# Kernel optimization log

Hardware: AMD Instinct MI355X
Metric: run time of the kernel (lower is better)

The kernel has to match this reference:

```python
import jax, jax.numpy as jnp
import numpy as np

B, LQ, LK = 4, 512, 512
QS, KS, H, DV = 512, 512, 256, 512


def setup_inputs() -> dict:
    key = jax.random.key(0)
    ks = jax.random.split(key, 9)
    s_q = 1.0 / np.sqrt(QS)
    s_k = 1.0 / np.sqrt(KS)
    s_v = 1.0 / np.sqrt(H)
    return {
        "query": jax.random.normal(ks[0], (B, LQ, QS), jnp.float32),
        "key": jax.random.normal(ks[1], (B, LK, KS), jnp.float32),
        "value": jax.random.normal(ks[2], (B, LK, DV), jnp.float32),
        "wq": jax.random.uniform(ks[3], (H, QS), jnp.float32, -s_q, s_q),
        "bq": jax.random.uniform(ks[4], (H,), jnp.float32, -s_q, s_q),
        "wk": jax.random.uniform(ks[5], (H, KS), jnp.float32, -s_k, s_k),
        "bk": jax.random.uniform(ks[6], (H,), jnp.float32, -s_k, s_k),
        "wv": jax.random.uniform(ks[7], (H,), jnp.float32, -s_v, s_v),
        "bv": jax.random.uniform(ks[8], (), jnp.float32, -s_v, s_v),
    }


def reference(query, key, value, wq, bq, wk, bk, wv, bv):
    # q: [B, Lq, H], k: [B, Lk, H]
    q = jnp.einsum('bqd,hd->bqh', query, wq) + bq
    k = jnp.einsum('bkd,hd->bkh', key, wk) + bk
    # broadcast add -> [B, Lq, Lk, H], tanh, project to scalar score
    feats = jnp.tanh(q[:, :, None, :] + k[:, None, :, :])
    scores = jnp.einsum('bqkh,h->bqk', feats, wv) + bv  # [B, Lq, Lk]
    attn = jax.nn.softmax(scores, axis=-1)
    # dropout p=0.0 (identity at inference)
    return jnp.einsum('bqk,bkd->bqd', attn, value)
```

## Files before the change

### kernel.cpp

```cpp
#include <hip/hip_runtime.h>

#define LOG2E 1.4426950408889634f

constexpr int Bb = 4, LQ = 512, LK = 512, QS = 512, H = 256, DV = 512;
constexpr int M = 2048;

constexpr size_t OFF_EQT = 0;
constexpr size_t OFF_EKT = 2u << 20;
constexpr size_t OFF_PQ  = 4u << 20;
constexpr size_t OFF_ROW = 6u << 20;
constexpr size_t OFF_VT  = 8u << 20;

using bf16x8 = __attribute__((ext_vector_type(8))) short;
using f32x4v = __attribute__((ext_vector_type(4))) float;

__device__ inline unsigned short f2bf(float x) {
    unsigned int u = __float_as_uint(x);
    u += 0x7FFFu + ((u >> 16) & 1u);
    return (unsigned short)(u >> 16);
}
__device__ inline unsigned int pk2(float lo, float hi) {
    unsigned int r;
    asm("v_cvt_pk_bf16_f32 %0, %1, %2" : "=v"(r) : "v"(lo), "v"(hi));
    return r;
}

__global__ __launch_bounds__(512) void proj_mfma(
    const float* __restrict__ query, const float* __restrict__ key,
    const float* __restrict__ wq, const float* __restrict__ wk,
    const float* __restrict__ bq, const float* __restrict__ bk,
    char* __restrict__ ws, float scale)
{
    const int z = blockIdx.z;
    const float* A    = z ? key : query;
    const float* W    = z ? wk : wq;
    const float* bias = z ? bk : bq;
    float* out = (float*)(ws + (z ? OFF_EKT : OFF_EQT));
    const float off = z ? 0.0f : 13.0f;

    __shared__ unsigned short Als[64][136];
    __shared__ unsigned short Wls[64][136];
    __shared__ float Ot[64][68];

    const int mb = blockIdx.x * 64, nb = blockIdx.y * 64;
    const int tid = threadIdx.x;
    const int wid = tid >> 6, lane = tid & 63;
    const int ml = lane & 15, quad = lane >> 4;
    const int ms = wid & 3, nh = wid >> 2;

    f32x4v acc0 = {0, 0, 0, 0}, acc1 = {0, 0, 0, 0};

    for (int kc = 0; kc < QS; kc += 128) {
        __syncthreads();
#pragma unroll
        for (int it = 0; it < 2; ++it) {
            int u = tid + it * 512;
            int row = u >> 4, c8 = (u & 15) * 8;
            float4 a0 = *(const float4*)(A + (size_t)(mb + row) * 512 + kc + c8);
            float4 a1 = *(const float4*)(A + (size_t)(mb + row) * 512 + kc + c8 + 4);
            uint4 pa = { pk2(a0.x, a0.y), pk2(a0.z, a0.w), pk2(a1.x, a1.y), pk2(a1.z, a1.w) };
            *(uint4*)&Als[row][c8] = pa;
            float4 w0 = *(const float4*)(W + (size_t)(nb + row) * 512 + kc + c8);
            float4 w1 = *(const float4*)(W + (size_t)(nb + row) * 512 + kc + c8 + 4);
            uint4 pw = { pk2(w0.x, w0.y), pk2(w0.z, w0.w), pk2(w1.x, w1.y), pk2(w1.z, w1.w) };
            *(uint4*)&Wls[row][c8] = pw;
        }
        __syncthreads();
#pragma unroll
        for (int s = 0; s < 4; ++s) {
            int k = s * 32 + quad * 8;
            bf16x8 af = *(const bf16x8*)&Als[ms * 16 + ml][k];
            bf16x8 b0 = *(const bf16x8*)&Wls[(nh * 2 + 0) * 16 + ml][k];
            bf16x8 b1 = *(const bf16x8*)&Wls[(nh * 2 + 1) * 16 + ml][k];
            acc0 = __builtin_amdgcn_mfma_f32_16x16x32_bf16(af, b0, acc0, 0, 0, 0);
            acc1 = __builtin_amdgcn_mfma_f32_16x16x32_bf16(af, b1, acc1, 0, 0, 0);
        }
    }

    __syncthreads();
#pragma unroll
    for (int r = 0; r < 4; ++r) {
        Ot[(nh * 2 + 0) * 16 + ml][ms * 16 + quad * 4 + r] = acc0[r];
        Ot[(nh * 2 + 1) * 16 + ml][ms * 16 + quad * 4 + r] = acc1[r];
    }
    __syncthreads();
    {
        int r0 = tid >> 3;
        int c0 = (tid & 7) * 8;
        float bs = bias[nb + r0];
#pragma unroll
        for (int g = 0; g < 2; ++g) {
            float4 v = *(const float4*)&Ot[r0][c0 + g * 4];
            float4 o;
            o.x = __builtin_amdgcn_exp2f(fminf(fmaxf(scale * (v.x + bs), -13.f), 13.f) - off);
            o.y = __builtin_amdgcn_exp2f(fminf(fmaxf(scale * (v.y + bs), -13.f), 13.f) - off);
            o.z = __builtin_amdgcn_exp2f(fminf(fmaxf(scale * (v.z + bs), -13.f), 13.f) - off);
            o.w = __builtin_amdgcn_exp2f(fminf(fmaxf(scale * (v.w + bs), -13.f), 13.f) - off);
            *(float4*)(out + (size_t)(nb + r0) * 2048 + mb + c0 + g * 4) = o;
        }
    }
}

__global__ __launch_bounds__(256) void vconv(
    const float* __restrict__ V, char* __restrict__ ws)
{
    unsigned short* VT = (unsigned short*)(ws + OFF_VT);
    __shared__ unsigned short T[64][72];
    const int b = blockIdx.z, k0 = blockIdx.x * 64, n0 = blockIdx.y * 64;
    const int tid = threadIdx.x;
    const float* Vb = V + (size_t)b * 512 * 512;
    const int r = tid >> 4, c = (tid & 15) * 4;
#pragma unroll
    for (int it = 0; it < 4; ++it) {
        int kr = r + it * 16;
        float4 v = *(const float4*)(Vb + (size_t)(k0 + kr) * 512 + n0 + c);
        T[c + 0][kr] = f2bf(v.x);
        T[c + 1][kr] = f2bf(v.y);
        T[c + 2][kr] = f2bf(v.z);
        T[c + 3][kr] = f2bf(v.w);
    }
    __syncthreads();
    const int rowO = tid >> 3, colO = (tid & 7) * 8;
#pragma unroll
    for (int it = 0; it < 2; ++it) {
        int n = rowO + it * 32;
        uint4 o = *(const uint4*)&T[n][colO];
        *(uint4*)(VT + ((size_t)b * 512 + n0 + n) * 512 + k0 + colO) = o;
    }
}

__global__ __launch_bounds__(512, 4) void score_kernel(
    const float* __restrict__ wvp, char* __restrict__ ws)
{
    const float* EqT = (const float*)(ws + OFF_EQT);
    const float* EkT = (const float*)(ws + OFF_EKT);
    unsigned short* Pq = (unsigned short*)(ws + OFF_PQ);
    float* rowpart = (float*)(ws + OFF_ROW);

    __shared__ float Qs[64][32];
    __shared__ float Ks[64][64];
    __shared__ float Wv2[H];
    __shared__ float redS[8][32];

    const int b  = blockIdx.z;
    const int qb = blockIdx.x * 32;
    const int kt = blockIdx.y;
    const int kb = kt * 64;
    const int tid = threadIdx.x;
    const int tx = tid & 15;
    const int ty = tid >> 4;
    const int w  = tid >> 6;
    const int lane = tid & 63;

    constexpr float S = 0.0001220703125f;
    if (tid < H) Wv2[tid] = wvp[tid] * (2.0f * LOG2E) * S;

    const int mq = b * LQ + qb;
    const int mk = b * LK + kb;

    float acc[2][2] = {};

    for (int h0 = 0; h0 < H; h0 += 64) {
        __syncthreads();
        {
            int hq = tid >> 3, cq = (tid & 7) * 4;
            *(float4*)&Qs[hq][cq] = *(const float4*)(EqT + (size_t)(h0 + hq) * M + mq + cq);
            int hk = tid >> 4, ck = (tid & 15) * 4;
            *(float4*)&Ks[hk][ck]      = *(const float4*)(EkT + (size_t)(h0 + hk) * M + mk + ck);
            *(float4*)&Ks[hk + 32][ck] = *(const float4*)(EkT + (size_t)(h0 + hk + 32) * M + mk + ck);
        }
        __syncthreads();
#pragma unroll 2
        for (int hh = 0; hh < 64; hh += 8) {
            float2 qv[8], kv[8];
#pragma unroll
            for (int u = 0; u < 8; ++u) qv[u] = *(const float2*)&Qs[hh + u][tx * 2];
#pragma unroll
            for (int u = 0; u < 8; ++u) kv[u] = *(const float2*)&Ks[hh + u][ty * 2];
            const float4 wA = *(const float4*)&Wv2[h0 + hh];
            const float4 wB = *(const float4*)&Wv2[h0 + hh + 4];
#pragma unroll
            for (int i = 0; i < 2; ++i)
#pragma unroll
                for (int j = 0; j < 2; ++j) {
                    float t[8];
#pragma unroll
                    for (int u = 0; u < 8; ++u)
                        t[u] = fmaf(i ? qv[u].y : qv[u].x, j ? kv[u].y : kv[u].x, S);
                    float t12 = t[0] * t[1], t34 = t[2] * t[3];
                    float n12 = fmaf(wA.x, t[1], wA.y * t[0]);
                    float n34 = fmaf(wA.z, t[3], wA.w * t[2]);
                    float numA = fmaf(n12, t34, n34 * t12);
                    float denA = t12 * t34;
                    float t56 = t[4] * t[5], t78 = t[6] * t[7];
                    float m12 = fmaf(wB.x, t[5], wB.y * t[4]);
                    float m34 = fmaf(wB.z, t[7], wB.w * t[6]);
                    float numB = fmaf(m12, t78, m34 * t56);
                    float denB = t56 * t78;
                    float NUMv = fmaf(numA, denB, numB * denA);
                    float DENv = denA * denB;
                    acc[i][j] = fmaf(NUMv, __builtin_amdgcn_rcpf(DENv), acc[i][j]);
                }
        }
    }

    float ps[2];
#pragma unroll
    for (int i = 0; i < 2; ++i) {
        int q = qb + tx * 2 + i;
        float p0 = __builtin_amdgcn_exp2f(-acc[i][0]);
        float p1 = __builtin_amdgcn_exp2f(-acc[i][1]);
        ps[i] = p0 + p1;
        *(unsigned int*)(Pq + ((size_t)(b * 512 + q) * 512 + kb + ty * 2)) = pk2(p0, p1);
    }
#pragma unroll
    for (int i = 0; i < 2; ++i) {
        ps[i] += __shfl_xor(ps[i], 16, 64);
        ps[i] += __shfl_xor(ps[i], 32, 64);
    }
    if (lane < 16) {
#pragma unroll
        for (int i = 0; i < 2; ++i) redS[w][tx * 2 + i] = ps[i];
    }
    __syncthreads();
    if (tid < 32) {
        float s = ((redS[0][tid] + redS[1][tid]) + (redS[2][tid] + redS[3][tid]))
                + ((redS[4][tid] + redS[5][tid]) + (redS[6][tid] + redS[7][tid]));
        rowpart[(size_t)kt * 2048 + b * 512 + qb + tid] = s;
    }
}

__global__ __launch_bounds__(512, 2) void av_mfma(
    const char* __restrict__ wsc, float* __restrict__ O)
{
    const unsigned short* Pq = (const unsigned short*)(wsc + OFF_PQ);
    const unsigned short* VT = (const unsigned short*)(wsc + OFF_VT);
    const float* rowpart = (const float*)(wsc + OFF_ROW);

    __shared__ unsigned short Pls[64][136];
    __shared__ unsigned short Vls[64][136];

    const int b = blockIdx.z, qb = blockIdx.x * 64, nb = blockIdx.y * 64;
    const int tid = threadIdx.x;
    const int wid = tid >> 6, lane = tid & 63;
    const int ml = lane & 15, quad = lane >> 4;
    const int ms = wid & 3, nh = wid >> 2;
    const unsigned short* Pb = Pq + (size_t)b * 512 * 512;
    const unsigned short* Vb = VT + (size_t)b * 512 * 512;

    f32x4v acc[2] = {{0,0,0,0},{0,0,0,0}};

    for (int kc = 0; kc < LK; kc += 128) {
        __syncthreads();
#pragma unroll
        for (int it = 0; it < 2; ++it) {
            int u = tid + it * 512;
            int row = u >> 4, c8 = (u & 15) * 8;
            *(uint4*)&Pls[row][c8] = *(const uint4*)(Pb + (size_t)(qb + row) * 512 + kc + c8);
            *(uint4*)&Vls[row][c8] = *(const uint4*)(Vb + (size_t)(nb + row) * 512 + kc + c8);
        }
        __syncthreads();
#pragma unroll
        for (int s = 0; s < 4; ++s) {
            int k = s * 32 + quad * 8;
            bf16x8 af = *(const bf16x8*)&Pls[ms * 16 + ml][k];
#pragma unroll
            for (int t = 0; t < 2; ++t) {
                bf16x8 bfr = *(const bf16x8*)&Vls[(nh * 2 + t) * 16 + ml][k];
                acc[t] = __builtin_amdgcn_mfma_f32_16x16x32_bf16(af, bfr, acc[t], 0, 0, 0);
            }
        }
    }

    float rr[4];
#pragma unroll
    for (int r = 0; r < 4; ++r) {
        int q = qb + ms * 16 + quad * 4 + r;
        float rs = 0.f;
#pragma unroll
        for (int t8 = 0; t8 < 8; ++t8) rs += rowpart[(size_t)t8 * 2048 + b * 512 + q];
        rr[r] = 1.0f / rs;
    }
#pragma unroll
    for (int t = 0; t < 2; ++t)
#pragma unroll
        for (int r = 0; r < 4; ++r) {
            int q = qb + ms * 16 + quad * 4 + r;
            O[((size_t)b * 512 + q) * 512 + nb + (nh * 2 + t) * 16 + ml] = acc[t][r] * rr[r];
        }
}

extern "C" void kernel_launch(void* const* d_in, const int* in_sizes, int n_in,
                              void* d_out, int out_size, void* d_ws, size_t ws_size,
                              hipStream_t stream) {
    const float* query = (const float*)d_in[0];
    const float* key   = (const float*)d_in[1];
    const float* value = (const float*)d_in[2];
    const float* wq    = (const float*)d_in[3];
    const float* bq    = (const float*)d_in[4];
    const float* wk    = (const float*)d_in[5];
    const float* bk    = (const float*)d_in[6];
    const float* wv    = (const float*)d_in[7];
    float* out = (float*)d_out;
    char* ws = (char*)d_ws;

    const float c2 = 2.0f * LOG2E;

    proj_mfma<<<dim3(32, 4, 2), 512, 0, stream>>>(query, key, wq, wk, bq, bk, ws, c2);
    vconv<<<dim3(8, 8, Bb), 256, 0, stream>>>(value, ws);
    score_kernel<<<dim3(16, 8, Bb), 512, 0, stream>>>(wv, ws);
    av_mfma<<<dim3(8, 8, Bb), 512, 0, stream>>>(ws, out);
}
```

Before: 118.4 us.

## Merge V conversion into projection kernel and prefetch tiles through registers

Folds the value transpose and bf16 conversion into the projection launch as a third grid slice, dropping one kernel launch. It also adds register prefetching of the next K-chunk in the projection and AV GEMM loops, plus double-buffered LDS with a register prefetch in the score kernel, so global loads overlap compute. The costs are higher register pressure, more LDS in the score kernel (which may lower occupancy), and a union-shared layout for the merged kernel.

```diff
diff --git a/kernel.cpp b/kernel.cpp
--- a/kernel.cpp
+++ b/kernel.cpp
@@ -25,63 +25,111 @@
     return r;
 }
 
-__global__ __launch_bounds__(512) void proj_mfma(
+__global__ __launch_bounds__(512, 4) void proj_vconv(
     const float* __restrict__ query, const float* __restrict__ key,
     const float* __restrict__ wq, const float* __restrict__ wk,
     const float* __restrict__ bq, const float* __restrict__ bk,
-    char* __restrict__ ws, float scale)
+    const float* __restrict__ V, char* __restrict__ ws, float scale)
 {
+    union Sh {
+        struct {
+            unsigned short Als[64][136];
+            unsigned short Wls[64][136];
+            float Ot[64][68];
+        } p;
+        unsigned short T[128][72];
+    };
+    __shared__ Sh sh;
+
+    const int tid = threadIdx.x;
     const int z = blockIdx.z;
+
+    if (z == 2) {
+        unsigned short* VT = (unsigned short*)(ws + OFF_VT);
+        const int id = blockIdx.y * 32 + blockIdx.x;
+        const int b = id >> 5;
+        const int t32 = id & 31;
+        const int k0 = (t32 & 7) * 64, n0 = (t32 >> 3) * 128;
+        const float* Vb = V + (size_t)b * 512 * 512;
+        const int r = tid >> 5, c = (tid & 31) * 4;
+#pragma unroll
+        for (int it = 0; it < 4; ++it) {
+            int kr = r + it * 16;
+            float4 v = *(const float4*)(Vb + (size_t)(k0 + kr) * 512 + n0 + c);
+            sh.T[c + 0][kr] = f2bf(v.x);
+            sh.T[c + 1][kr] = f2bf(v.y);
+            sh.T[c + 2][kr] = f2bf(v.z);
+            sh.T[c + 3][kr] = f2bf(v.w);
+        }
+        __syncthreads();
+        const int rowO = tid >> 2, colO = (tid & 3) * 16;
+        uint4 o0 = *(const uint4*)&sh.T[rowO][colO];
+        uint4 o1 = *(const uint4*)&sh.T[rowO][colO + 8];
+        unsigned short* dst = VT + ((size_t)b * 512 + n0 + rowO) * 512 + k0 + colO;
+        *(uint4*)(dst)     = o0;
+        *(uint4*)(dst + 8) = o1;
+        return;
+    }
+
     const float* A    = z ? key : query;
     const float* W    = z ? wk : wq;
     const float* bias = z ? bk : bq;
     float* out = (float*)(ws + (z ? OFF_EKT : OFF_EQT));
     const float off = z ? 0.0f : 13.0f;
 
-    __shared__ unsigned short Als[64][136];
-    __shared__ unsigned short Wls[64][136];
-    __shared__ float Ot[64][68];
-
     const int mb = blockIdx.x * 64, nb = blockIdx.y * 64;
-    const int tid = threadIdx.x;
     const int wid = tid >> 6, lane = tid & 63;
     const int ml = lane & 15, quad = lane >> 4;
     const int ms = wid & 3, nh = wid >> 2;
 
     f32x4v acc0 = {0, 0, 0, 0}, acc1 = {0, 0, 0, 0};
 
+    float4 ra0[2], ra1[2], rw0[2], rw1[2];
+    const int row0 = tid >> 4, c80 = (tid & 15) * 8;
+    const int row1 = (tid + 512) >> 4, c81 = c80;
+#define PROJ_LOAD(KC)                                                          \
+    {                                                                          \
+        ra0[0] = *(const float4*)(A + (size_t)(mb + row0) * 512 + (KC) + c80); \
+        ra1[0] = *(const float4*)(A + (size_t)(mb + row0) * 512 + (KC) + c80 + 4); \
+        rw0[0] = *(const float4*)(W + (size_t)(nb + row0) * 512 + (KC) + c80); \
+        rw1[0] = *(const float4*)(W + (size_t)(nb + row0) * 512 + (KC) + c80 + 4); \
+        ra0[1] = *(const float4*)(A + (size_t)(mb + row1) * 512 + (KC) + c81); \
+        ra1[1] = *(const float4*)(A + (size_t)(mb + row1) * 512 + (KC) + c81 + 4); \
+        rw0[1] = *(const float4*)(W + (size_t)(nb + row1) * 512 + (KC) + c81); \
+        rw1[1] = *(const float4*)(W + (size_t)(nb + row1) * 512 + (KC) + c81 + 4); \
+    }
+
+    PROJ_LOAD(0);
     for (int kc = 0; kc < QS; kc += 128) {
-        __syncthreads();
 #pragma unroll
         for (int it = 0; it < 2; ++it) {
-            int u = tid + it * 512;
-            int row = u >> 4, c8 = (u & 15) * 8;
-            float4 a0 = *(const float4*)(A + (size_t)(mb + row) * 512 + kc + c8);
-            float4 a1 = *(const float4*)(A + (size_t)(mb + row) * 512 + kc + c8 + 4);
-            uint4 pa = { pk2(a0.x, a0.y), pk2(a0.z, a0.w), pk2(a1.x, a1.y), pk2(a1.z, a1.w) };
-            *(uint4*)&Als[row][c8] = pa;
-            float4 w0 = *(const float4*)(W + (size_t)(nb + row) * 512 + kc + c8);
-            float4 w1 = *(const float4*)(W + (size_t)(nb + row) * 512 + kc + c8 + 4);
-            uint4 pw = { pk2(w0.x, w0.y), pk2(w0.z, w0.w), pk2(w1.x, w1.y), pk2(w1.z, w1.w) };
-            *(uint4*)&Wls[row][c8] = pw;
-        }
-        __syncthreads();
+            int row = it ? row1 : row0;
+            uint4 pa = { pk2(ra0[it].x, ra0[it].y), pk2(ra0[it].z, ra0[it].w),
+                         pk2(ra1[it].x, ra1[it].y), pk2(ra1[it].z, ra1[it].w) };
+            *(uint4*)&sh.p.Als[row][c80] = pa;
+            uint4 pw = { pk2(rw0[it].x, rw0[it].y), pk2(rw0[it].z, rw0[it].w),
+                         pk2(rw1[it].x, rw1[it].y), pk2(rw1[it].z, rw1[it].w) };
+            *(uint4*)&sh.p.Wls[row][c80] = pw;
+        }
+        __syncthreads();
+        if (kc < QS - 128) PROJ_LOAD(kc + 128);
 #pragma unroll
         for (int s = 0; s < 4; ++s) {
             int k = s * 32 + quad * 8;
-            bf16x8 af = *(const bf16x8*)&Als[ms * 16 + ml][k];
-            bf16x8 b0 = *(const bf16x8*)&Wls[(nh * 2 + 0) * 16 + ml][k];
-            bf16x8 b1 = *(const bf16x8*)&Wls[(nh * 2 + 1) * 16 + ml][k];
+            bf16x8 af = *(const bf16x8*)&sh.p.Als[ms * 16 + ml][k];
+            bf16x8 b0 = *(const bf16x8*)&sh.p.Wls[(nh * 2 + 0) * 16 + ml][k];
+            bf16x8 b1 = *(const bf16x8*)&sh.p.Wls[(nh * 2 + 1) * 16 + ml][k];
             acc0 = __builtin_amdgcn_mfma_f32_16x16x32_bf16(af, b0, acc0, 0, 0, 0);
             acc1 = __builtin_amdgcn_mfma_f32_16x16x32_bf16(af, b1, acc1, 0, 0, 0);
         }
-    }
-
-    __syncthreads();
+        __syncthreads();
+    }
+#undef PROJ_LOAD
+
 #pragma unroll
     for (int r = 0; r < 4; ++r) {
-        Ot[(nh * 2 + 0) * 16 + ml][ms * 16 + quad * 4 + r] = acc0[r];
-        Ot[(nh * 2 + 1) * 16 + ml][ms * 16 + quad * 4 + r] = acc1[r];
+        sh.p.Ot[(nh * 2 + 0) * 16 + ml][ms * 16 + quad * 4 + r] = acc0[r];
+        sh.p.Ot[(nh * 2 + 1) * 16 + ml][ms * 16 + quad * 4 + r] = acc1[r];
     }
     __syncthreads();
     {
@@ -90,7 +138,7 @@
         float bs = bias[nb + r0];
 #pragma unroll
         for (int g = 0; g < 2; ++g) {
-            float4 v = *(const float4*)&Ot[r0][c0 + g * 4];
+            float4 v = *(const float4*)&sh.p.Ot[r0][c0 + g * 4];
             float4 o;
             o.x = __builtin_amdgcn_exp2f(fminf(fmaxf(scale * (v.x + bs), -13.f), 13.f) - off);
             o.y = __builtin_amdgcn_exp2f(fminf(fmaxf(scale * (v.y + bs), -13.f), 13.f) - off);
@@ -98,34 +146,6 @@
             o.w = __builtin_amdgcn_exp2f(fminf(fmaxf(scale * (v.w + bs), -13.f), 13.f) - off);
             *(float4*)(out + (size_t)(nb + r0) * 2048 + mb + c0 + g * 4) = o;
         }
-    }
-}
-
-__global__ __launch_bounds__(256) void vconv(
-    const float* __restrict__ V, char* __restrict__ ws)
-{
-    unsigned short* VT = (unsigned short*)(ws + OFF_VT);
-    __shared__ unsigned short T[64][72];
-    const int b = blockIdx.z, k0 = blockIdx.x * 64, n0 = blockIdx.y * 64;
-    const int tid = threadIdx.x;
-    const float* Vb = V + (size_t)b * 512 * 512;
-    const int r = tid >> 4, c = (tid & 15) * 4;
-#pragma unroll
-    for (int it = 0; it < 4; ++it) {
-        int kr = r + it * 16;
-        float4 v = *(const float4*)(Vb + (size_t)(k0 + kr) * 512 + n0 + c);
-        T[c + 0][kr] = f2bf(v.x);
-        T[c + 1][kr] = f2bf(v.y);
-        T[c + 2][kr] = f2bf(v.z);
-        T[c + 3][kr] = f2bf(v.w);
-    }
-    __syncthreads();
-    const int rowO = tid >> 3, colO = (tid & 7) * 8;
-#pragma unroll
-    for (int it = 0; it < 2; ++it) {
-        int n = rowO + it * 32;
-        uint4 o = *(const uint4*)&T[n][colO];
-        *(uint4*)(VT + ((size_t)b * 512 + n0 + n) * 512 + k0 + colO) = o;
     }
 }
 
@@ -137,8 +157,8 @@
     unsigned short* Pq = (unsigned short*)(ws + OFF_PQ);
     float* rowpart = (float*)(ws + OFF_ROW);
 
-    __shared__ float Qs[64][32];
-    __shared__ float Ks[64][64];
+    __shared__ float Qs[2][64][32];
+    __shared__ float Ks[2][64][64];
     __shared__ float Wv2[H];
     __shared__ float redS[8][32];
 
@@ -157,50 +177,66 @@
 
     const int mq = b * LQ + qb;
     const int mk = b * LK + kb;
+    const int hq = tid >> 3, cq = (tid & 7) * 4;
+    const int hk = tid >> 4, ck = (tid & 15) * 4;
+
+    float4 pq, pk0, pk1;
+    pq  = *(const float4*)(EqT + (size_t)hq * M + mq + cq);
+    pk0 = *(const float4*)(EkT + (size_t)hk * M + mk + ck);
+    pk1 = *(const float4*)(EkT + (size_t)(hk + 32) * M + mk + ck);
+    *(float4*)&Qs[0][hq][cq]      = pq;
+    *(float4*)&Ks[0][hk][ck]      = pk0;
+    *(float4*)&Ks[0][hk + 32][ck] = pk1;
 
     float acc[2][2] = {};
 
-    for (int h0 = 0; h0 < H; h0 += 64) {
-        __syncthreads();
-        {
-            int hq = tid >> 3, cq = (tid & 7) * 4;
-            *(float4*)&Qs[hq][cq] = *(const float4*)(EqT + (size_t)(h0 + hq) * M + mq + cq);
-            int hk = tid >> 4, ck = (tid & 15) * 4;
-            *(float4*)&Ks[hk][ck]      = *(const float4*)(EkT + (size_t)(h0 + hk) * M + mk + ck);
-            *(float4*)&Ks[hk + 32][ck] = *(const float4*)(EkT + (size_t)(h0 + hk + 32) * M + mk + ck);
-        }
-        __syncthreads();
+    for (int t = 0; t < 4; ++t) {
+        __syncthreads();
+        if (t < 3) {
+            int h0n = (t + 1) * 64;
+            pq  = *(const float4*)(EqT + (size_t)(h0n + hq) * M + mq + cq);
+            pk0 = *(const float4*)(EkT + (size_t)(h0n + hk) * M + mk + ck);
+            pk1 = *(const float4*)(EkT + (size_t)(h0n + hk + 32) * M + mk + ck);
+        }
+        const int h0 = t * 64;
+        const int cb = t & 1;
 #pragma unroll 2
         for (int hh = 0; hh < 64; hh += 8) {
             float2 qv[8], kv[8];
 #pragma unroll
-            for (int u = 0; u < 8; ++u) qv[u] = *(const float2*)&Qs[hh + u][tx * 2];
-#pragma unroll
-            for (int u = 0; u < 8; ++u) kv[u] = *(const float2*)&Ks[hh + u][ty * 2];
+            for (int u = 0; u < 8; ++u) qv[u] = *(const float2*)&Qs[cb][hh + u][tx * 2];
+#pragma unroll
+            for (int u = 0; u < 8; ++u) kv[u] = *(const float2*)&Ks[cb][hh + u][ty * 2];
             const float4 wA = *(const float4*)&Wv2[h0 + hh];
             const float4 wB = *(const float4*)&Wv2[h0 + hh + 4];
 #pragma unroll
             for (int i = 0; i < 2; ++i)
 #pragma unroll
                 for (int j = 0; j < 2; ++j) {
-                    float t[8];
+                    float t8a[8];
 #pragma unroll
                     for (int u = 0; u < 8; ++u)
-                        t[u] = fmaf(i ? qv[u].y : qv[u].x, j ? kv[u].y : kv[u].x, S);
-                    float t12 = t[0] * t[1], t34 = t[2] * t[3];
-                    float n12 = fmaf(wA.x, t[1], wA.y * t[0]);
-                    float n34 = fmaf(wA.z, t[3], wA.w * t[2]);
+                        t8a[u] = fmaf(i ? qv[u].y : qv[u].x, j ? kv[u].y : kv[u].x, S);
+                    float t12 = t8a[0] * t8a[1], t34 = t8a[2] * t8a[3];
+                    float n12 = fmaf(wA.x, t8a[1], wA.y * t8a[0]);
+                    float n34 = fmaf(wA.z, t8a[3], wA.w * t8a[2]);
                     float numA = fmaf(n12, t34, n34 * t12);
                     float denA = t12 * t34;
-                    float t56 = t[4] * t[5], t78 = t[6] * t[7];
-                    float m12 = fmaf(wB.x, t[5], wB.y * t[4]);
-                    float m34 = fmaf(wB.z, t[7], wB.w * t[6]);
+                    float t56 = t8a[4] * t8a[5], t78 = t8a[6] * t8a[7];
+                    float m12 = fmaf(wB.x, t8a[5], wB.y * t8a[4]);
+                    float m34 = fmaf(wB.z, t8a[7], wB.w * t8a[6]);
                     float numB = fmaf(m12, t78, m34 * t56);
                     float denB = t56 * t78;
                     float NUMv = fmaf(numA, denB, numB * denA);
                     float DENv = denA * denB;
                     acc[i][j] = fmaf(NUMv, __builtin_amdgcn_rcpf(DENv), acc[i][j]);
                 }
+        }
+        if (t < 3) {
+            const int nb2 = (t + 1) & 1;
+            *(float4*)&Qs[nb2][hq][cq]      = pq;
+            *(float4*)&Ks[nb2][hk][ck]      = pk0;
+            *(float4*)&Ks[nb2][hk + 32][ck] = pk1;
         }
     }
 
@@ -248,18 +284,28 @@
     const unsigned short* Pb = Pq + (size_t)b * 512 * 512;
     const unsigned short* Vb = VT + (size_t)b * 512 * 512;
 
+    const int row0 = tid >> 4, c80 = (tid & 15) * 8;
+    const int row1 = (tid + 512) >> 4;
+
+    uint4 rp[2], rv[2];
+#define AV_LOAD(KC)                                                            \
+    {                                                                          \
+        rp[0] = *(const uint4*)(Pb + (size_t)(qb + row0) * 512 + (KC) + c80);  \
+        rv[0] = *(const uint4*)(Vb + (size_t)(nb + row0) * 512 + (KC) + c80);  \
+        rp[1] = *(const uint4*)(Pb + (size_t)(qb + row1) * 512 + (KC) + c80);  \
+        rv[1] = *(const uint4*)(Vb + (size_t)(nb + row1) * 512 + (KC) + c80);  \
+    }
+
     f32x4v acc[2] = {{0,0,0,0},{0,0,0,0}};
 
+    AV_LOAD(0);
     for (int kc = 0; kc < LK; kc += 128) {
-        __syncthreads();
-#pragma unroll
-        for (int it = 0; it < 2; ++it) {
-            int u = tid + it * 512;
-            int row = u >> 4, c8 = (u & 15) * 8;
-            *(uint4*)&Pls[row][c8] = *(const uint4*)(Pb + (size_t)(qb + row) * 512 + kc + c8);
-            *(uint4*)&Vls[row][c8] = *(const uint4*)(Vb + (size_t)(nb + row) * 512 + kc + c8);
-        }
-        __syncthreads();
+        *(uint4*)&Pls[row0][c80] = rp[0];
+        *(uint4*)&Vls[row0][c80] = rv[0];
+        *(uint4*)&Pls[row1][c80] = rp[1];
+        *(uint4*)&Vls[row1][c80] = rv[1];
+        __syncthreads();
+        if (kc < LK - 128) AV_LOAD(kc + 128);
 #pragma unroll
         for (int s = 0; s < 4; ++s) {
             int k = s * 32 + quad * 8;
@@ -270,7 +316,9 @@
                 acc[t] = __builtin_amdgcn_mfma_f32_16x16x32_bf16(af, bfr, acc[t], 0, 0, 0);
             }
         }
-    }
+        __syncthreads();
+    }
+#undef AV_LOAD
 
     float rr[4];
 #pragma unroll
@@ -306,8 +354,7 @@
 
     const float c2 = 2.0f * LOG2E;
 
-    proj_mfma<<<dim3(32, 4, 2), 512, 0, stream>>>(query, key, wq, wk, bq, bk, ws, c2);
-    vconv<<<dim3(8, 8, Bb), 256, 0, stream>>>(value, ws);
+    proj_vconv<<<dim3(32, 4, 3), 512, 0, stream>>>(query, key, wq, wk, bq, bk, value, ws, c2);
     score_kernel<<<dim3(16, 8, Bb), 512, 0, stream>>>(wv, ws);
     av_mfma<<<dim3(8, 8, Bb), 512, 0, stream>>>(ws, out);
 }
```

Measured after the change: 125.5 us. +6.1%, slower.
